# Kernel optimization log

Hardware: AMD Instinct MI355X
Metric: run time of the kernel (lower is better)

## Reference

```python
import jax, jax.numpy as jnp
import numpy as np

B, C, H, W = 4, 64, 96, 96
KS, NH = 7, 4


def setup_inputs() -> dict:
    key = jax.random.key(0)
    ks = jax.random.split(key, 9)
    s = 0.1  # keep logits in a sane range for softmax
    return {
        "input_x": jax.random.normal(ks[0], (B, C, H, W), jnp.float32),
        "q_w": jax.random.normal(ks[1], (C, C), jnp.float32) * s,
        "q_b": jax.random.normal(ks[2], (C,), jnp.float32) * s,
        "k_w": jax.random.normal(ks[3], (C, C), jnp.float32) * s,
        "k_b": jax.random.normal(ks[4], (C,), jnp.float32) * s,
        "v_w": jax.random.normal(ks[5], (C, C), jnp.float32) * s,
        "v_b": jax.random.normal(ks[6], (C,), jnp.float32) * s,
        "rel_h": jax.random.normal(ks[7], (C // 2, KS, 1), jnp.float32) * s,
        "rel_w": jax.random.normal(ks[8], (C // 2, 1, KS), jnp.float32) * s,
    }


def _unfold(x, ks):
    # x: (B, C, Hp, Wp) -> (B, C, Ho, Wo, ks, ks), same as torch .unfold(2).unfold(3)
    Hp, Wp = x.shape[2], x.shape[3]
    Ho, Wo = Hp - ks + 1, Wp - ks + 1
    ih = jnp.arange(Ho)[:, None] + jnp.arange(ks)[None, :]  # (Ho, ks)
    iw = jnp.arange(Wo)[:, None] + jnp.arange(ks)[None, :]  # (Wo, ks)
    return x[:, :, ih[:, None, :, None], iw[None, :, None, :]]


def reference(input_x, q_w, q_b, k_w, k_b, v_w, v_b, rel_h, rel_w):
    b, c, h, w = input_x.shape
    ks, nh = KS, NH
    dkh = c // nh
    p0 = (ks - 1) // 2
    p1 = ks - 1 - p0
    padded = jnp.pad(input_x, ((0, 0), (0, 0), (p0, p1), (p0, p1)))

    conv1x1 = lambda x, wt, bi: jnp.einsum('bchw,oc->bohw', x, wt) + bi[None, :, None, None]
    k = conv1x1(padded, k_w, k_b)
    v = conv1x1(padded, v_w, v_b)
    q = conv1x1(input_x, q_w, q_b)

    # flat reshapes exactly as in torch (row-major), reproducing its layout semantics
    k = _unfold(k, ks).reshape(b, nh, h, w, dkh, ks * ks)
    v = _unfold(v, ks).reshape(b, nh, h, w, dkh, ks * ks)
    q = q.reshape(b, nh, h, w, dkh)  # torch: (b,nh,h,w,dkh,1) squeezed

    qk = jnp.einsum('bnxyd,bnxydk->bnxyk', q, k).reshape(b, nh, h, w, ks, ks)
    # torch einsum 'bhxydz,cij->bhxyij' == (sum_d q) outer (sum_c rel)
    qsum = q.sum(-1)  # (b, nh, h, w)
    rel = rel_h.sum(0) + rel_w.sum(0)  # broadcasts to (ks, ks)
    qk = qk + qsum[..., None, None] * rel

    weights = jax.nn.softmax(qk.reshape(b, nh, h, w, ks * ks), axis=-1)
    attn = jnp.einsum('bnxyk,bnxydk->bnxyd', weights, v)  # (b, nh, h, w, dkh)
    attn = attn.reshape(b, c, h, w)  # flat reshape, matching torch
    return jax.nn.relu(attn)
```

## Files before the change

### kernel.cpp

```cpp
#include <hip/hip_runtime.h>

#define B_ 4
#define C_ 64
#define H_ 96
#define W_ 96
#define KS_ 7
#define PH_ 102
#define PSTR 104
#define LDSTR 108


__global__ __launch_bounds__(128) void qkv_conv_kernel(
    const float* __restrict__ in,
    const float* __restrict__ qw, const float* __restrict__ qb,
    const float* __restrict__ kw, const float* __restrict__ kb,
    const float* __restrict__ vw, const float* __restrict__ vb,
    float* __restrict__ outq, float* __restrict__ outk, float* __restrict__ outv)
{
    const int mz    = blockIdx.z;
    const int mode  = mz >> 2;
    const int obase = (mz & 3) * 16;
    const int b     = blockIdx.y;
    const int p     = blockIdx.x * 128 + threadIdx.x;

    int h, wc;
    bool inb;
    const float* w;
    const float* bi;
    float* op;
    size_t ostr;

    if (mode == 0) {
        if (p >= H_ * W_) return;
        h = p / W_; wc = p - h * W_;
        inb = true;
        w = qw; bi = qb;
        op = outq + ((size_t)b * C_ + obase) * H_ * W_ + (size_t)h * W_ + wc;
        ostr = (size_t)H_ * W_;
    } else {
        if (p >= PH_ * PH_) return;
        const int ph = p / PH_, pw = p - ph * PH_;
        h = ph - 3; wc = pw - 3;
        inb = (h >= 0 && h < H_ && wc >= 0 && wc < W_);
        w  = (mode == 1) ? kw : vw;
        bi = (mode == 1) ? kb : vb;
        op = ((mode == 1) ? outk : outv)
           + ((size_t)b * C_ + obase) * PH_ * PSTR + (size_t)ph * PSTR + pw;
        ostr = (size_t)PH_ * PSTR;
    }

    float x[C_];
    if (inb) {
        const float* ip = in + (size_t)b * C_ * H_ * W_ + (size_t)h * W_ + wc;
        #pragma unroll
        for (int c = 0; c < C_; ++c) x[c] = ip[(size_t)c * H_ * W_];
    } else {
        #pragma unroll
        for (int c = 0; c < C_; ++c) x[c] = 0.f;
    }

    #pragma unroll 1
    for (int r = 0; r < 2; ++r) {
        const int ob = obase + r * 8;
        float acc[8];
        #pragma unroll
        for (int t = 0; t < 8; ++t) acc[t] = bi[ob + t];
        #pragma unroll
        for (int c = 0; c < C_; ++c) {
            #pragma unroll
            for (int t = 0; t < 8; ++t)
                acc[t] = fmaf(w[(ob + t) * C_ + c], x[c], acc[t]);
        }
        #pragma unroll
        for (int t = 0; t < 8; ++t) op[(size_t)(r * 8 + t) * ostr] = acc[t];
    }
}

__global__ __launch_bounds__(384) void attn_kernel(
    const float* __restrict__ q, const float* __restrict__ k,
    const float* __restrict__ v, const float* __restrict__ relh,
    const float* __restrict__ relw, float* __restrict__ out)
{
    const int bx   = blockIdx.x;
    const int tile = bx % 3;
    const int c    = (bx / 3) % C_;
    const int b    = bx / (3 * C_);
    const int ho0  = tile * 32;
    const int t    = threadIdx.x;

    __shared__ float ks[38 * LDSTR];
    __shared__ float vs[38 * LDSTR];
    __shared__ float rel_s[49];

    if (t < 49) {
        const int i = t / KS_, j = t % KS_;
        float s = 0.f;
        #pragma unroll
        for (int cc = 0; cc < C_ / 2; ++cc)
            s += relh[cc * KS_ + i] + relw[cc * KS_ + j];
        rel_s[t] = s;
    }

    {
        const float* kp = k + ((size_t)(b * C_ + c) * PH_ + ho0) * PSTR;
        const float* vp = v + ((size_t)(b * C_ + c) * PH_ + ho0) * PSTR;
        for (int idx = t; idx < 38 * 26; idx += 384) {
            const int r = idx / 26, col = (idx % 26) * 4;
            *reinterpret_cast<float4*>(&ks[r * LDSTR + col]) =
                *reinterpret_cast<const float4*>(kp + r * PSTR + col);
            *reinterpret_cast<float4*>(&vs[r * LDSTR + col]) =
                *reinterpret_cast<const float4*>(vp + r * PSTR + col);
        }
    }
    __syncthreads();

    const int r0   = t / 12;
    const int rest = t % 12;
    const int w0b  = rest >> 1;
    const int half = rest & 1;
    const int w0   = w0b * 16;
    const int ho   = ho0 + r0;

    const float* qp = q + (((size_t)b * C_ + c) * H_ + ho) * W_ + w0;
    float qs[16];
    #pragma unroll
    for (int tt = 0; tt < 16; tt += 4) {
        float4 f = *reinterpret_cast<const float4*>(qp + tt);
        qs[tt] = f.x; qs[tt + 1] = f.y; qs[tt + 2] = f.z; qs[tt + 3] = f.w;
    }
    float qsum = 0.f;
    #pragma unroll
    for (int tt = 0; tt < 16; ++tt) qsum += qs[tt];

    float logit[49];
    #pragma unroll
    for (int i = 0; i < KS_; ++i) {
        float kr[22];
        const float* kp = &ks[(r0 + i) * LDSTR + w0];
        #pragma unroll
        for (int tt = 0; tt < 20; tt += 4) {
            float4 f = *reinterpret_cast<const float4*>(kp + tt);
            kr[tt] = f.x; kr[tt + 1] = f.y; kr[tt + 2] = f.z; kr[tt + 3] = f.w;
        }
        float2 f2 = *reinterpret_cast<const float2*>(kp + 20);
        kr[20] = f2.x; kr[21] = f2.y;
        #pragma unroll
        for (int j = 0; j < KS_; ++j) {
            float s = 0.f;
            #pragma unroll
            for (int tt = 0; tt < 16; ++tt) s = fmaf(qs[tt], kr[tt + j], s);
            logit[i * KS_ + j] = s + qsum * rel_s[i * KS_ + j];
        }
    }

    float m = -1e30f;
    #pragma unroll
    for (int kk = 0; kk < 49; ++kk) m = fmaxf(m, logit[kk]);
    float ssum = 0.f;
    #pragma unroll
    for (int kk = 0; kk < 49; ++kk) {
        float e = __expf(logit[kk] - m);
        logit[kk] = e;
        ssum += e;
    }
    const float inv = 1.f / ssum;

    float o8[8];
    #pragma unroll
    for (int d = 0; d < 8; ++d) o8[d] = 0.f;

    #pragma unroll
    for (int i = 0; i < KS_; ++i) {
        float vr[14];
        const float* vp = &vs[(r0 + i) * LDSTR + w0 + half * 8];
        #pragma unroll
        for (int tt = 0; tt < 12; tt += 4) {
            float4 f = *reinterpret_cast<const float4*>(vp + tt);
            vr[tt] = f.x; vr[tt + 1] = f.y; vr[tt + 2] = f.z; vr[tt + 3] = f.w;
        }
        float2 f2 = *reinterpret_cast<const float2*>(vp + 12);
        vr[12] = f2.x; vr[13] = f2.y;
        #pragma unroll
        for (int j = 0; j < KS_; ++j) {
            float wgt = logit[i * KS_ + j];
            #pragma unroll
            for (int d = 0; d < 8; ++d) o8[d] = fmaf(wgt, vr[d + j], o8[d]);
        }
    }

    float* op = out + (((size_t)b * C_ + c) * H_ + ho) * W_ + w0 + half * 8;
    #pragma unroll
    for (int d = 0; d < 8; d += 4) {
        float4 f;
        f.x = fmaxf(o8[d]     * inv, 0.f);
        f.y = fmaxf(o8[d + 1] * inv, 0.f);
        f.z = fmaxf(o8[d + 2] * inv, 0.f);
        f.w = fmaxf(o8[d + 3] * inv, 0.f);
        *reinterpret_cast<float4*>(op + d) = f;
    }
}

extern "C" void kernel_launch(void* const* d_in, const int* in_sizes, int n_in,
                              void* d_out, int out_size, void* d_ws, size_t ws_size,
                              hipStream_t stream) {
    const float* in   = (const float*)d_in[0];
    const float* qw   = (const float*)d_in[1];
    const float* qb   = (const float*)d_in[2];
    const float* kw   = (const float*)d_in[3];
    const float* kb   = (const float*)d_in[4];
    const float* vw   = (const float*)d_in[5];
    const float* vb   = (const float*)d_in[6];
    const float* relh = (const float*)d_in[7];
    const float* relw = (const float*)d_in[8];
    float* out = (float*)d_out;

    float* wk = (float*)d_ws;
    float* wv = wk + (size_t)B_ * C_ * PH_ * PSTR;
    float* wq = wv + (size_t)B_ * C_ * PH_ * PSTR;

    dim3 cgrid((PH_ * PH_ + 127) / 128, B_, 12);
    qkv_conv_kernel<<<cgrid, 128, 0, stream>>>(in, qw, qb, kw, kb, vw, vb, wq, wk, wv);

    dim3 agrid(B_ * C_ * 3);
    attn_kernel<<<agrid, 384, 0, stream>>>(wq, wk, wv, relh, relw, out);
}
```

Measured before the change: 46.59 us.

## Compute QKV 1x1 convolutions with bf16 MFMA and separate border fill

Replaces the scalar FP32 per-pixel QKV convolution with a bf16 MFMA GEMM. Each block stages 64 pixels of input as bf16 in a swizzled LDS tile and computes all 192 output channels. A prep kernel converts the weights to bf16, gathers the biases, and writes bias values into the padded borders of K and V, so the main conv only touches interior pixels. The aim is to cut FP32 FMA work and the redundant input reloads across the 12 z-slices. In exchange it adds an extra launch and lowers precision to bf16 inputs, which may exceed tolerance.

Result: faster. 41.88 us (-10.1%).

```diff
diff --git a/kernel.cpp b/kernel.cpp
--- a/kernel.cpp
+++ b/kernel.cpp
@@ -7,72 +7,152 @@
 #define KS_ 7
 #define PH_ 102
 #define PSTR 104
+#define PHW (PH_ * PSTR)
+#define NPIX (H_ * W_)
 #define LDSTR 108
 
-
-__global__ __launch_bounds__(128) void qkv_conv_kernel(
-    const float* __restrict__ in,
+typedef __attribute__((ext_vector_type(8))) short short8;
+typedef __attribute__((ext_vector_type(4))) float f32x4;
+
+static __device__ inline ushort f2bf(float f) {
+    union { float f; unsigned u; } v; v.f = f;
+    unsigned r = (v.u + 0x7fff + ((v.u >> 16) & 1)) >> 16;
+    return (ushort)r;
+}
+
+
+__global__ __launch_bounds__(256) void prep_kernel(
     const float* __restrict__ qw, const float* __restrict__ qb,
     const float* __restrict__ kw, const float* __restrict__ kb,
     const float* __restrict__ vw, const float* __restrict__ vb,
+    ushort* __restrict__ wbf, float* __restrict__ bias_all,
+    float* __restrict__ outk, float* __restrict__ outv)
+{
+    const int gid = blockIdx.x * 256 + threadIdx.x;
+    if (blockIdx.x < 48) {
+        const int idx = gid;
+        const float* src = (idx < 4096) ? qw : (idx < 8192 ? kw : vw);
+        wbf[idx] = f2bf(src[idx & 4095]);
+        if (idx < 192) {
+            const float* bsrc = (idx < 64) ? qb : (idx < 128 ? kb : vb);
+            bias_all[idx] = bsrc[idx & 63];
+        }
+        return;
+    }
+    int item = gid - 48 * 256;
+    if (item >= B_ * 2 * C_ * 1188) return;
+    const int bp   = item % 1188;
+    int rest       = item / 1188;
+    const int ch   = rest % C_;
+    rest /= C_;
+    const int mode = rest & 1;
+    const int b    = rest >> 1;
+    int ph, pw;
+    if (bp < 306)      { ph = bp / 102;              pw = bp % 102; }
+    else if (bp < 612) { int j = bp - 306; ph = 99 + j / 102; pw = j % 102; }
+    else               { int j = bp - 612; ph = 3 + j / 6; int c2 = j % 6;
+                         pw = (c2 < 3) ? c2 : 96 + c2 - 3 + 3; }
+    const float bias = (mode ? vb : kb)[ch];
+    float* dst = mode ? outv : outk;
+    dst[((size_t)b * C_ + ch) * PHW + ph * PSTR + pw] = bias;
+}
+
+__global__ __launch_bounds__(256) void mfma_conv_kernel(
+    const float* __restrict__ in,
+    const ushort* __restrict__ wbf,
+    const float* __restrict__ bias_all,
     float* __restrict__ outq, float* __restrict__ outk, float* __restrict__ outv)
 {
-    const int mz    = blockIdx.z;
-    const int mode  = mz >> 2;
-    const int obase = (mz & 3) * 16;
-    const int b     = blockIdx.y;
-    const int p     = blockIdx.x * 128 + threadIdx.x;
-
-    int h, wc;
-    bool inb;
-    const float* w;
-    const float* bi;
-    float* op;
-    size_t ostr;
-
-    if (mode == 0) {
-        if (p >= H_ * W_) return;
-        h = p / W_; wc = p - h * W_;
-        inb = true;
-        w = qw; bi = qb;
-        op = outq + ((size_t)b * C_ + obase) * H_ * W_ + (size_t)h * W_ + wc;
-        ostr = (size_t)H_ * W_;
-    } else {
-        if (p >= PH_ * PH_) return;
-        const int ph = p / PH_, pw = p - ph * PH_;
-        h = ph - 3; wc = pw - 3;
-        inb = (h >= 0 && h < H_ && wc >= 0 && wc < W_);
-        w  = (mode == 1) ? kw : vw;
-        bi = (mode == 1) ? kb : vb;
-        op = ((mode == 1) ? outk : outv)
-           + ((size_t)b * C_ + obase) * PH_ * PSTR + (size_t)ph * PSTR + pw;
-        ostr = (size_t)PH_ * PSTR;
-    }
-
-    float x[C_];
-    if (inb) {
-        const float* ip = in + (size_t)b * C_ * H_ * W_ + (size_t)h * W_ + wc;
-        #pragma unroll
-        for (int c = 0; c < C_; ++c) x[c] = ip[(size_t)c * H_ * W_];
-    } else {
-        #pragma unroll
-        for (int c = 0; c < C_; ++c) x[c] = 0.f;
-    }
-
-    #pragma unroll 1
-    for (int r = 0; r < 2; ++r) {
-        const int ob = obase + r * 8;
-        float acc[8];
-        #pragma unroll
-        for (int t = 0; t < 8; ++t) acc[t] = bi[ob + t];
-        #pragma unroll
-        for (int c = 0; c < C_; ++c) {
+    const int b    = blockIdx.y;
+    const int pix0 = blockIdx.x * 64;
+    const int t    = threadIdx.x;
+    const int lane = t & 63;
+    const int wv   = t >> 6;
+
+    __shared__ ushort xs[64 * 64];
+
+    {
+        const int pix = t & 63;
+        const int cg  = t >> 6;
+        const float* xp = in + (size_t)b * C_ * NPIX + pix0 + pix;
+        #pragma unroll
+        for (int g = 0; g < 4; ++g) {
+            const int ch = (cg + 4 * g) * 4;
+            float x0 = xp[(size_t)(ch    ) * NPIX];
+            float x1 = xp[(size_t)(ch + 1) * NPIX];
+            float x2 = xp[(size_t)(ch + 2) * NPIX];
+            float x3 = xp[(size_t)(ch + 3) * NPIX];
+            ushort4 u = make_ushort4(f2bf(x0), f2bf(x1), f2bf(x2), f2bf(x3));
+            unsigned byte = (unsigned)(pix * 128 + ch * 2) ^ (unsigned)((pix & 7) << 4);
+            *reinterpret_cast<ushort4*>(reinterpret_cast<char*>(xs) + byte) = u;
+        }
+    }
+    __syncthreads();
+
+    short8 afr[3][2];
+    #pragma unroll
+    for (int i = 0; i < 3; ++i) {
+        const int row = (3 * wv + i) * 16 + (lane & 15);
+        #pragma unroll
+        for (int ka = 0; ka < 2; ++ka) {
+            const int kk = ka * 32 + (lane >> 4) * 8;
+            afr[i][ka] = *reinterpret_cast<const short8*>(wbf + row * 64 + kk);
+        }
+    }
+    short8 bfr[4][2];
+    #pragma unroll
+    for (int nt = 0; nt < 4; ++nt) {
+        const int pl = nt * 16 + (lane & 15);
+        #pragma unroll
+        for (int ka = 0; ka < 2; ++ka) {
+            const int kk = ka * 32 + (lane >> 4) * 8;
+            unsigned byte = (unsigned)(pl * 128 + kk * 2) ^ (unsigned)((pl & 7) << 4);
+            bfr[nt][ka] = *reinterpret_cast<const short8*>(
+                reinterpret_cast<const char*>(xs) + byte);
+        }
+    }
+    f32x4 acc[3][4];
+    #pragma unroll
+    for (int i = 0; i < 3; ++i) {
+        const int mt = 3 * wv + i;
+        f32x4 bi;
+        #pragma unroll
+        for (int r = 0; r < 4; ++r) bi[r] = bias_all[mt * 16 + (lane >> 4) * 4 + r];
+        #pragma unroll
+        for (int nt = 0; nt < 4; ++nt) acc[i][nt] = bi;
+    }
+    #pragma unroll
+    for (int i = 0; i < 3; ++i) {
+        #pragma unroll
+        for (int nt = 0; nt < 4; ++nt) {
+            acc[i][nt] = __builtin_amdgcn_mfma_f32_16x16x32_bf16(
+                afr[i][0], bfr[nt][0], acc[i][nt], 0, 0, 0);
+            acc[i][nt] = __builtin_amdgcn_mfma_f32_16x16x32_bf16(
+                afr[i][1], bfr[nt][1], acc[i][nt], 0, 0, 0);
+        }
+    }
+    #pragma unroll
+    for (int nt = 0; nt < 4; ++nt) {
+        const int pix  = pix0 + nt * 16 + (lane & 15);
+        const int h    = pix / 96;
+        const int w    = pix - h * 96;
+        const int ppix = (h + 3) * PSTR + (w + 3);
+        #pragma unroll
+        for (int i = 0; i < 3; ++i) {
+            const int mt   = 3 * wv + i;
+            const int mode = mt >> 2;
+            const int ocb  = (mt & 3) * 16 + (lane >> 4) * 4;
             #pragma unroll
-            for (int t = 0; t < 8; ++t)
-                acc[t] = fmaf(w[(ob + t) * C_ + c], x[c], acc[t]);
-        }
-        #pragma unroll
-        for (int t = 0; t < 8; ++t) op[(size_t)(r * 8 + t) * ostr] = acc[t];
+            for (int r = 0; r < 4; ++r) {
+                const float val = acc[i][nt][r];
+                if (mode == 0)
+                    outq[((size_t)b * C_ + ocb + r) * NPIX + pix] = val;
+                else if (mode == 1)
+                    outk[((size_t)b * C_ + ocb + r) * PHW + ppix] = val;
+                else
+                    outv[((size_t)b * C_ + ocb + r) * PHW + ppix] = val;
+            }
+        }
     }
 }
 
@@ -100,7 +180,6 @@
             s += relh[cc * KS_ + i] + relw[cc * KS_ + j];
         rel_s[t] = s;
     }
-
     {
         const float* kp = k + ((size_t)(b * C_ + c) * PH_ + ho0) * PSTR;
         const float* vp = v + ((size_t)(b * C_ + c) * PH_ + ho0) * PSTR;
@@ -116,9 +195,8 @@
 
     const int r0   = t / 12;
     const int rest = t % 12;
-    const int w0b  = rest >> 1;
+    const int w0   = (rest >> 1) * 16;
     const int half = rest & 1;
-    const int w0   = w0b * 16;
     const int ho   = ho0 + r0;
 
     const float* qp = q + (((size_t)b * C_ + c) * H_ + ho) * W_ + w0;
@@ -214,13 +292,18 @@
     const float* relw = (const float*)d_in[8];
     float* out = (float*)d_out;
 
-    float* wk = (float*)d_ws;
-    float* wv = wk + (size_t)B_ * C_ * PH_ * PSTR;
-    float* wq = wv + (size_t)B_ * C_ * PH_ * PSTR;
-
-    dim3 cgrid((PH_ * PH_ + 127) / 128, B_, 12);
-    qkv_conv_kernel<<<cgrid, 128, 0, stream>>>(in, qw, qb, kw, kb, vw, vb, wq, wk, wv);
+    float*  wk  = (float*)d_ws;
+    float*  wvv = wk  + (size_t)B_ * C_ * PHW;
+    float*  wq  = wvv + (size_t)B_ * C_ * PHW;
+    ushort* wbf = (ushort*)(wq + (size_t)B_ * C_ * NPIX);
+    float*  wbias = (float*)(wbf + 192 * 64);
+
+    prep_kernel<<<48 + 2376, 256, 0, stream>>>(qw, qb, kw, kb, vw, vb,
+                                               wbf, wbias, wk, wvv);
+
+    dim3 cgrid(NPIX / 64, B_);
+    mfma_conv_kernel<<<cgrid, 256, 0, stream>>>(in, wbf, wbias, wq, wk, wvv);
 
     dim3 agrid(B_ * C_ * 3);
-    attn_kernel<<<agrid, 384, 0, stream>>>(wq, wk, wv, relh, relw, out);
-}
+    attn_kernel<<<agrid, 384, 0, stream>>>(wq, wk, wvv, relh, relw, out);
+}
```
